# Optimization experiments

Measured on AMD Instinct MI355X. Metric: run time of the kernel, lower is better.

The kernel has to match this reference:

```python
import jax, jax.numpy as jnp
import numpy as np

B, N, K = 64, 128, 12
D_ATOM, D_NBR, D_NEW = 256, 320, 256
H, DK = 8, 32  # D_NEW = H * DK
LN_EPS = 1e-5
NEG_INF = -1e9


def setup_inputs() -> dict:
    key = jax.random.key(0)
    ks = jax.random.split(key, 10)
    atom_feature = jax.random.normal(ks[0], (B, N, D_ATOM), jnp.float32)
    atom_neighbor_feature = jax.random.normal(ks[1], (B, N, K, D_NBR), jnp.float32)
    # valid-neighbor masks from random neighbor counts in [1, K]
    counts = jax.random.randint(ks[2], (B, N), 1, K + 1)
    valid = (jnp.arange(K)[None, None, :] < counts[:, :, None]).astype(jnp.float32)
    atom_attend_mask = valid[..., None]                      # (B,N,K,1), 1=real neighbor
    atom_softmax_mask = (1.0 - valid[..., None]) * NEG_INF   # (B,N,K,1), additive
    # parameters
    s = 1.0 / np.sqrt(D_ATOM)
    W_atom = jax.random.uniform(ks[3], (D_ATOM, D_NEW), jnp.float32, -s, s)
    b_atom = jnp.zeros((D_NEW,), jnp.float32)
    s2 = 1.0 / np.sqrt(D_NBR)
    W_nbr = jax.random.uniform(ks[4], (D_NBR, D_NEW), jnp.float32, -s2, s2)
    b_nbr = jnp.zeros((D_NEW,), jnp.float32)
    s3 = 1.0 / np.sqrt(DK)
    w_align = jax.random.uniform(ks[5], (DK, 1), jnp.float32, -s3, s3)
    b_align = jnp.zeros((1,), jnp.float32)
    ln_gamma = jnp.ones((D_NEW,), jnp.float32)
    ln_beta = jnp.zeros((D_NEW,), jnp.float32)
    return dict(atom_feature=atom_feature, atom_neighbor_feature=atom_neighbor_feature,
                atom_softmax_mask=atom_softmax_mask, atom_attend_mask=atom_attend_mask,
                W_atom=W_atom, b_atom=b_atom, W_nbr=W_nbr, b_nbr=b_nbr,
                w_align=w_align, b_align=b_align, ln_gamma=ln_gamma, ln_beta=ln_beta)


def reference(atom_feature, atom_neighbor_feature, atom_softmax_mask, atom_attend_mask,
              W_atom, b_atom, W_nbr, b_nbr, w_align, b_align, ln_gamma, ln_beta):
    # dropout is identity at eval time
    h = atom_feature @ W_atom + b_atom                    # (B,N,D_NEW)
    e = atom_neighbor_feature @ W_nbr + b_nbr             # (B,N,K,D_NEW)
    h = h.reshape(B, N, 1, H, DK)                         # broadcast over K
    e = e.reshape(B, N, K, H, DK)
    # GATv2: act(h_i + e_j) then per-head linear score
    feat = jax.nn.leaky_relu(h + e)                       # slope 0.01 == torch default
    score = feat @ w_align + b_align                      # (B,N,K,H,1)
    score = score + atom_softmax_mask[:, :, :, None, :]   # additive -inf on pad
    attn = jax.nn.softmax(score, axis=2)                  # softmax over neighbors K
    attn = attn * atom_attend_mask[:, :, :, None, :]
    ctx = jnp.sum(attn * e, axis=2).reshape(B, N, H * DK)  # (B,N,D_NEW)
    # LayerNorm
    mu = jnp.mean(ctx, axis=-1, keepdims=True)
    xc = ctx - mu
    var = jnp.mean(xc * xc, axis=-1, keepdims=True)
    return xc * jax.lax.rsqrt(var + LN_EPS) * ln_gamma + ln_beta
```

## Files before the change

### kernel.cpp

```cpp
#include <hip/hip_runtime.h>

#define KN 12
#define DNBR 320
#define DNEW 256
#define BN_TOT 8192
#define ATB 4
#define HATB 16
#define NKS_E 10
#define NKS_H 8
#define ASTR_H 264
#define H_OFF 294912

typedef short bf8_t __attribute__((ext_vector_type(8)));
typedef float f32x4 __attribute__((ext_vector_type(4)));
typedef unsigned short us8 __attribute__((ext_vector_type(8)));
using u16 = unsigned short;
using u32 = unsigned int;

typedef __attribute__((address_space(3))) void lds_vp;
typedef __attribute__((address_space(1))) const void gc_vp;

__device__ __forceinline__ void dma16(const void* g, void* l) {
    __builtin_amdgcn_global_load_lds((gc_vp*)g, (lds_vp*)l, 16, 0, 0);
}

__device__ __forceinline__ u16 f2bf(float f) {
    u32 x = __float_as_uint(f);
    return (u16)((x + 0x7fffu + ((x >> 16) & 1u)) >> 16);
}

__device__ __forceinline__ us8 pack8(float4 a, float4 b) {
    us8 v;
    v[0] = f2bf(a.x); v[1] = f2bf(a.y); v[2] = f2bf(a.z); v[3] = f2bf(a.w);
    v[4] = f2bf(b.x); v[5] = f2bf(b.y); v[6] = f2bf(b.z); v[7] = f2bf(b.w);
    return v;
}

__device__ __forceinline__ bf8_t cvt8(float4 a, float4 b) {
    u32 r0, r1, r2, r3;
    asm("v_cvt_pk_bf16_f32 %0, %1, %2" : "=v"(r0) : "v"(a.x), "v"(a.y));
    asm("v_cvt_pk_bf16_f32 %0, %1, %2" : "=v"(r1) : "v"(a.z), "v"(a.w));
    asm("v_cvt_pk_bf16_f32 %0, %1, %2" : "=v"(r2) : "v"(b.x), "v"(b.y));
    asm("v_cvt_pk_bf16_f32 %0, %1, %2" : "=v"(r3) : "v"(b.z), "v"(b.w));
    union { u32 u[4]; bf8_t v; } cv;
    cv.u[0] = r0; cv.u[1] = r1; cv.u[2] = r2; cv.u[3] = r3;
    return cv.v;
}

__global__ __launch_bounds__(256) void build_b2(
    const float* __restrict__ Wn, const float* __restrict__ Wa,
    u16* __restrict__ B2)
{
    int tile = blockIdx.x * 4 + (threadIdx.x >> 6);
    int l = threadIdx.x & 63;
    int q = l >> 4, m = l & 15;
    us8 v;
    if (tile < 160) {
        int ks = tile >> 4, nt = tile & 15;
        int col = nt * 16 + m;
#pragma unroll
        for (int e = 0; e < 8; e++)
            v[e] = f2bf(Wn[(ks * 32 + q * 8 + e) * DNEW + col]);
    } else {
        int tt = tile - 160;
        int ks = tt >> 4, nt = tt & 15;
        int col = nt * 16 + m;
#pragma unroll
        for (int e = 0; e < 8; e++)
            v[e] = f2bf(Wa[(ks * 32 + q * 8 + e) * DNEW + col]);
    }
    *(us8*)&B2[(size_t)tile * 512 + l * 8] = v;
}

__global__ __launch_bounds__(256) void h_pre(
    const float* __restrict__ atomf, const u16* __restrict__ B2,
    const float* __restrict__ ba, float* __restrict__ h_g)
{
    __shared__ u16 A[HATB * ASTR_H];

    const int t = threadIdx.x;
    const int l = t & 63, w = t >> 6, q = l >> 4, m = l & 15;
    const int ab = blockIdx.x * HATB;

    const float* base = atomf + (size_t)ab * DNEW;
    float4 u0 = *(const float4*)(base + t * 8);
    float4 u1 = *(const float4*)(base + t * 8 + 4);
    float4 u2 = *(const float4*)(base + (t + 256) * 8);
    float4 u3 = *(const float4*)(base + (t + 256) * 8 + 4);
    int ai = t >> 5, c8 = t & 31;
    *(us8*)&A[ai * ASTR_H + c8 * 8] = pack8(u0, u1);
    *(us8*)&A[(ai + 8) * ASTR_H + c8 * 8] = pack8(u2, u3);
    __syncthreads();

    f32x4 acc[4];
#pragma unroll
    for (int j = 0; j < 4; j++) acc[j] = (f32x4){0.f, 0.f, 0.f, 0.f};

#pragma unroll
    for (int ks = 0; ks < NKS_H; ks++) {
        bf8_t af = *(bf8_t*)&A[m * ASTR_H + ks * 32 + q * 8];
#pragma unroll
        for (int j = 0; j < 4; j++) {
            bf8_t bfj = *(const bf8_t*)&B2[((size_t)(160 + ks * 16 + w * 4 + j) * 64 + l) * 8];
            acc[j] = __builtin_amdgcn_mfma_f32_16x16x32_bf16(af, bfj, acc[j], 0, 0, 0);
        }
    }
#pragma unroll
    for (int j = 0; j < 4; j++) {
        int col = w * 64 + j * 16 + m;
        float bav = ba[col];
#pragma unroll
        for (int r = 0; r < 4; r++) {
            int row = ab + q * 4 + r;
            h_g[(size_t)row * DNEW + col] = acc[j][r] + bav;
        }
    }
}

__global__ __launch_bounds__(256, 2) void fused_all(
    const float* __restrict__ nbrf,
    const float* __restrict__ smaskg, const float* __restrict__ amaskg,
    const u16* __restrict__ B2, const float* __restrict__ h_g,
    const float* __restrict__ bnb, const float* __restrict__ walg,
    const float* __restrict__ balg, const float* __restrict__ gam,
    const float* __restrict__ bet, float* __restrict__ out)
{
    __shared__ __align__(16) float smem[ATB * 20 * 256];

    const int t = threadIdx.x;
    const int l = t & 63, q = l >> 4, m = l & 15;
    const int w = t >> 6;
    const int atom = blockIdx.x * ATB + w;
    const bool qv = (q < 3);

    const int cc = l >> 4;
    const int srow = (m < KN) ? m : (KN - 1);
    const float* abase = nbrf + ((size_t)atom * KN + srow) * DNBR;
    char* lbase = (char*)smem + (size_t)w * 20480;
#pragma unroll
    for (int c = 0; c < 20; c++) {
        int ks = c >> 1, h = c & 1;
        dma16(abase + ks * 32 + h * 16 + cc * 4, lbase + c * 1024);
    }

    const float bal = balg[0];
    float hv[16], bnbv[16];
#pragma unroll
    for (int j = 0; j < 16; j++) {
        int col = j * 16 + m;
        hv[j] = h_g[(size_t)atom * DNEW + col];
        bnbv[j] = bnb[col];
    }
    float wv2[2] = { walg[m], walg[16 + m] };
    float smv[4], amv[4];
#pragma unroll
    for (int r = 0; r < 4; r++) {
        int k = q * 4 + r;
        smv[r] = qv ? smaskg[(size_t)atom * KN + k] + bal : 0.f;
        amv[r] = qv ? amaskg[(size_t)atom * KN + k] : 0.f;
    }

    asm volatile("s_waitcnt vmcnt(0)" ::: "memory");
    __builtin_amdgcn_sched_barrier(0);

    const float4* A2w = (const float4*)lbase;
    const bf8_t* B2v = (const bf8_t*)B2;
    const int aoff = (q & 1) * 32 + m;
    const int hsel = q >> 1;

    f32x4 acc[16];
#pragma unroll
    for (int j = 0; j < 16; j++) acc[j] = (f32x4){0.f, 0.f, 0.f, 0.f};

#pragma unroll
    for (int ks = 0; ks < NKS_E; ks++) {
        bf8_t bfj[16];
#pragma unroll
        for (int j = 0; j < 16; j++)
            bfj[j] = B2v[(size_t)(ks * 16 + j) * 64 + l];
        float4 lo = A2w[(ks * 2 + hsel) * 64 + aoff];
        float4 hi = A2w[(ks * 2 + hsel) * 64 + aoff + 16];
        bf8_t af = cvt8(lo, hi);
#pragma unroll
        for (int j = 0; j < 16; j++)
            acc[j] = __builtin_amdgcn_mfma_f32_16x16x32_bf16(af, bfj[j], acc[j], 0, 0, 0);
    }

#pragma unroll
    for (int j = 0; j < 16; j++)
#pragma unroll
        for (int r = 0; r < 4; r++) acc[j][r] += bnbv[j];

    float ctxv[16];
    float s1 = 0.f, s2 = 0.f;
#pragma unroll
    for (int u = 0; u < 8; u++) {
        const int j0 = 2 * u, j1 = 2 * u + 1;
        float p[4];
#pragma unroll
        for (int r = 0; r < 4; r++) {
            float pp = 0.f;
            float f0 = acc[j0][r] + hv[j0];
            f0 = f0 > 0.f ? f0 : 0.01f * f0;
            pp = fmaf(f0, wv2[0], pp);
            float f1 = acc[j1][r] + hv[j1];
            f1 = f1 > 0.f ? f1 : 0.01f * f1;
            pp = fmaf(f1, wv2[1], pp);
            pp += __shfl_xor(pp, 1);
            pp += __shfl_xor(pp, 2);
            pp += __shfl_xor(pp, 4);
            pp += __shfl_xor(pp, 8);
            p[r] = qv ? pp + smv[r] : -1e30f;
        }
        float mx = fmaxf(fmaxf(p[0], p[1]), fmaxf(p[2], p[3]));
        mx = fmaxf(mx, __shfl_xor(mx, 16));
        mx = fmaxf(mx, __shfl_xor(mx, 32));
        float ex[4], ss = 0.f;
#pragma unroll
        for (int r = 0; r < 4; r++) {
            ex[r] = qv ? __expf(p[r] - mx) : 0.f;
            ss += ex[r];
        }
        ss += __shfl_xor(ss, 16);
        ss += __shfl_xor(ss, 32);
        float inv = 1.f / ss;
        float am[4];
#pragma unroll
        for (int r = 0; r < 4; r++)
            am[r] = qv ? ex[r] * inv * amv[r] : 0.f;
#pragma unroll
        for (int jo = 0; jo < 2; jo++) {
            int j = 2 * u + jo;
            float cp = am[0] * acc[j][0] + am[1] * acc[j][1] +
                       am[2] * acc[j][2] + am[3] * acc[j][3];
            cp += __shfl_xor(cp, 16);
            cp += __shfl_xor(cp, 32);
            ctxv[j] = cp;
            s1 += cp;
            s2 += cp * cp;
        }
    }
#pragma unroll
    for (int off = 1; off < 16; off <<= 1) {
        s1 += __shfl_xor(s1, off);
        s2 += __shfl_xor(s2, off);
    }
    float mu = s1 * (1.f / 256.f);
    float var = s2 * (1.f / 256.f) - mu * mu;
    var = fmaxf(var, 0.f);
    float rs = rsqrtf(var + 1e-5f);

#pragma unroll
    for (int jj = 0; jj < 4; jj++) {
        int j = q * 4 + jj;
        int col = j * 16 + m;
        out[(size_t)atom * DNEW + col] =
            (ctxv[j] - mu) * rs * gam[col] + bet[col];
    }
}

extern "C" void kernel_launch(void* const* d_in, const int* in_sizes, int n_in,
                              void* d_out, int out_size, void* d_ws, size_t ws_size,
                              hipStream_t stream) {
    const float* atomf = (const float*)d_in[0];
    const float* nbrf  = (const float*)d_in[1];
    const float* smask = (const float*)d_in[2];
    const float* amask = (const float*)d_in[3];
    const float* Wa    = (const float*)d_in[4];
    const float* ba    = (const float*)d_in[5];
    const float* Wn    = (const float*)d_in[6];
    const float* bnb   = (const float*)d_in[7];
    const float* wal   = (const float*)d_in[8];
    const float* bal   = (const float*)d_in[9];
    const float* gam   = (const float*)d_in[10];
    const float* bet   = (const float*)d_in[11];
    float* outp = (float*)d_out;

    u16* B2 = (u16*)d_ws;
    float* h_g = (float*)((char*)d_ws + H_OFF);

    build_b2<<<72, 256, 0, stream>>>(Wn, Wa, B2);
    h_pre<<<BN_TOT / HATB, 256, 0, stream>>>(atomf, B2, ba, h_g);
    fused_all<<<BN_TOT / ATB, 256, 0, stream>>>(nbrf, smask, amask, B2, h_g,
                                                bnb, wal, bal, gam, bet, outp);
}
```

Measured before the change: 263.8 us.

## Split each atom's output columns across four waves, one atom per block

Previously each wave handled one whole atom (all 256 output columns, 16 accumulators). Now a block handles one atom, and each of its four waves computes 64 columns, so per-wave accumulators and B-fragment registers shrink by 4x. Launch bounds rise to allow 8 blocks per CU for higher occupancy. The LayerNorm statistics now need a cross-wave reduction through LDS with two extra __syncthreads. The change also adds block-level sync for the shared neighbor tile, and each wave now re-reads only its slice of the weights.

```diff
diff --git a/kernel.cpp b/kernel.cpp
--- a/kernel.cpp
+++ b/kernel.cpp
@@ -4,12 +4,12 @@
 #define DNBR 320
 #define DNEW 256
 #define BN_TOT 8192
-#define ATB 4
 #define HATB 16
 #define NKS_E 10
 #define NKS_H 8
 #define ASTR_H 264
 #define H_OFF 294912
+#define NCHUNK 20
 
 typedef short bf8_t __attribute__((ext_vector_type(8)));
 typedef float f32x4 __attribute__((ext_vector_type(4)));
@@ -117,7 +117,7 @@
     }
 }
 
-__global__ __launch_bounds__(256, 2) void fused_all(
+__global__ __launch_bounds__(256, 8) void fused_all(
     const float* __restrict__ nbrf,
     const float* __restrict__ smaskg, const float* __restrict__ amaskg,
     const u16* __restrict__ B2, const float* __restrict__ h_g,
@@ -125,33 +125,30 @@
     const float* __restrict__ balg, const float* __restrict__ gam,
     const float* __restrict__ bet, float* __restrict__ out)
 {
-    __shared__ __align__(16) float smem[ATB * 20 * 256];
+    __shared__ __align__(16) float smem[NCHUNK * 256];
 
     const int t = threadIdx.x;
-    const int l = t & 63, q = l >> 4, m = l & 15;
-    const int w = t >> 6;
-    const int atom = blockIdx.x * ATB + w;
+    const int l = t & 63, w = t >> 6, q = l >> 4, m = l & 15;
+    const int atom = blockIdx.x;
     const bool qv = (q < 3);
 
     const int cc = l >> 4;
     const int srow = (m < KN) ? m : (KN - 1);
     const float* abase = nbrf + ((size_t)atom * KN + srow) * DNBR;
-    char* lbase = (char*)smem + (size_t)w * 20480;
-#pragma unroll
-    for (int c = 0; c < 20; c++) {
+    for (int c = w; c < NCHUNK; c += 4) {
         int ks = c >> 1, h = c & 1;
-        dma16(abase + ks * 32 + h * 16 + cc * 4, lbase + c * 1024);
+        dma16(abase + ks * 32 + h * 16 + cc * 4, (char*)smem + (size_t)c * 1024);
     }
 
     const float bal = balg[0];
-    float hv[16], bnbv[16];
-#pragma unroll
-    for (int j = 0; j < 16; j++) {
-        int col = j * 16 + m;
+    float hv[4], bnbv[4], wv[4];
+#pragma unroll
+    for (int j = 0; j < 4; j++) {
+        int col = w * 64 + j * 16 + m;
         hv[j] = h_g[(size_t)atom * DNEW + col];
         bnbv[j] = bnb[col];
-    }
-    float wv2[2] = { walg[m], walg[16 + m] };
+        wv[j] = walg[(j * 16 + m) & 31];
+    }
     float smv[4], amv[4];
 #pragma unroll
     for (int r = 0; r < 4; r++) {
@@ -160,52 +157,51 @@
         amv[r] = qv ? amaskg[(size_t)atom * KN + k] : 0.f;
     }
 
-    asm volatile("s_waitcnt vmcnt(0)" ::: "memory");
-    __builtin_amdgcn_sched_barrier(0);
-
-    const float4* A2w = (const float4*)lbase;
+    __syncthreads();
+
+    const float4* A2 = (const float4*)smem;
     const bf8_t* B2v = (const bf8_t*)B2;
     const int aoff = (q & 1) * 32 + m;
     const int hsel = q >> 1;
 
-    f32x4 acc[16];
-#pragma unroll
-    for (int j = 0; j < 16; j++) acc[j] = (f32x4){0.f, 0.f, 0.f, 0.f};
+    f32x4 acc[4];
+#pragma unroll
+    for (int j = 0; j < 4; j++) acc[j] = (f32x4){0.f, 0.f, 0.f, 0.f};
 
 #pragma unroll
     for (int ks = 0; ks < NKS_E; ks++) {
-        bf8_t bfj[16];
-#pragma unroll
-        for (int j = 0; j < 16; j++)
-            bfj[j] = B2v[(size_t)(ks * 16 + j) * 64 + l];
-        float4 lo = A2w[(ks * 2 + hsel) * 64 + aoff];
-        float4 hi = A2w[(ks * 2 + hsel) * 64 + aoff + 16];
+        bf8_t bfj[4];
+#pragma unroll
+        for (int j = 0; j < 4; j++)
+            bfj[j] = B2v[(size_t)(ks * 16 + w * 4 + j) * 64 + l];
+        float4 lo = A2[(ks * 2 + hsel) * 64 + aoff];
+        float4 hi = A2[(ks * 2 + hsel) * 64 + aoff + 16];
         bf8_t af = cvt8(lo, hi);
 #pragma unroll
-        for (int j = 0; j < 16; j++)
+        for (int j = 0; j < 4; j++)
             acc[j] = __builtin_amdgcn_mfma_f32_16x16x32_bf16(af, bfj[j], acc[j], 0, 0, 0);
     }
 
 #pragma unroll
-    for (int j = 0; j < 16; j++)
+    for (int j = 0; j < 4; j++)
 #pragma unroll
         for (int r = 0; r < 4; r++) acc[j][r] += bnbv[j];
 
-    float ctxv[16];
+    float ctxv[4];
     float s1 = 0.f, s2 = 0.f;
 #pragma unroll
-    for (int u = 0; u < 8; u++) {
-        const int j0 = 2 * u, j1 = 2 * u + 1;
+    for (int jj = 0; jj < 2; jj++) {
         float p[4];
 #pragma unroll
         for (int r = 0; r < 4; r++) {
             float pp = 0.f;
-            float f0 = acc[j0][r] + hv[j0];
-            f0 = f0 > 0.f ? f0 : 0.01f * f0;
-            pp = fmaf(f0, wv2[0], pp);
-            float f1 = acc[j1][r] + hv[j1];
-            f1 = f1 > 0.f ? f1 : 0.01f * f1;
-            pp = fmaf(f1, wv2[1], pp);
+#pragma unroll
+            for (int jo = 0; jo < 2; jo++) {
+                int j = jj * 2 + jo;
+                float f = acc[j][r] + hv[j];
+                f = f > 0.f ? f : 0.01f * f;
+                pp = fmaf(f, wv[j], pp);
+            }
             pp += __shfl_xor(pp, 1);
             pp += __shfl_xor(pp, 2);
             pp += __shfl_xor(pp, 4);
@@ -230,7 +226,7 @@
             am[r] = qv ? ex[r] * inv * amv[r] : 0.f;
 #pragma unroll
         for (int jo = 0; jo < 2; jo++) {
-            int j = 2 * u + jo;
+            int j = jj * 2 + jo;
             float cp = am[0] * acc[j][0] + am[1] * acc[j][1] +
                        am[2] * acc[j][2] + am[3] * acc[j][3];
             cp += __shfl_xor(cp, 16);
@@ -245,17 +241,25 @@
         s1 += __shfl_xor(s1, off);
         s2 += __shfl_xor(s2, off);
     }
-    float mu = s1 * (1.f / 256.f);
-    float var = s2 * (1.f / 256.f) - mu * mu;
+
+    float* red_l = smem;
+    __syncthreads();
+    if (l == 0) { red_l[w] = s1; red_l[4 + w] = s2; }
+    __syncthreads();
+
+    float ts1 = red_l[0] + red_l[1] + red_l[2] + red_l[3];
+    float ts2 = red_l[4] + red_l[5] + red_l[6] + red_l[7];
+    float mu = ts1 * (1.f / 256.f);
+    float var = ts2 * (1.f / 256.f) - mu * mu;
     var = fmaxf(var, 0.f);
     float rs = rsqrtf(var + 1e-5f);
-
-#pragma unroll
-    for (int jj = 0; jj < 4; jj++) {
-        int j = q * 4 + jj;
-        int col = j * 16 + m;
-        out[(size_t)atom * DNEW + col] =
-            (ctxv[j] - mu) * rs * gam[col] + bet[col];
+    if (q == 0) {
+#pragma unroll
+        for (int j = 0; j < 4; j++) {
+            int col = w * 64 + j * 16 + m;
+            out[(size_t)atom * DNEW + col] =
+                (ctxv[j] - mu) * rs * gam[col] + bet[col];
+        }
     }
 }
 
@@ -281,6 +285,6 @@
 
     build_b2<<<72, 256, 0, stream>>>(Wn, Wa, B2);
     h_pre<<<BN_TOT / HATB, 256, 0, stream>>>(atomf, B2, ba, h_g);
-    fused_all<<<BN_TOT / ATB, 256, 0, stream>>>(nbrf, smask, amask, B2, h_g,
-                                                bnb, wal, bal, gam, bet, outp);
-}
+    fused_all<<<BN_TOT, 256, 0, stream>>>(nbrf, smask, amask, B2, h_g,
+                                          bnb, wal, bal, gam, bet, outp);
+}
```

After: 262.1 us. Within noise of the previous version (-0.7%).
